# Optimization experiments

Measured on AMD Instinct MI355X. Metric: run time of the kernel, lower is better.

The kernel has to match this reference:

```python
import jax, jax.numpy as jnp
import numpy as np

REG_STD = jnp.asarray([0.1, 0.1, 0.2, 0.2, 0.1], dtype=jnp.float32)  # normalize() target_std, mean=0


def setup_inputs() -> dict:
    key = jax.random.key(0)
    ks = jax.random.split(key, 8)
    B, N, C, R = 2, 2048, 256, 7
    D, H, NCLS = C * R * R, 1024, 10
    features = jax.random.normal(ks[0], (B, N, C, R, R), jnp.float32)
    boxes = jax.random.uniform(ks[1], (B, N, 5), jnp.float32)  # cx,cy,w,h,angle (stride units)
    strides = jnp.ones((B, N, 5), jnp.float32)
    W1 = jax.random.normal(ks[2], (D, H), jnp.float32) * 0.02
    b1 = jnp.zeros((H,), jnp.float32)
    W2 = jax.random.normal(ks[3], (H, H), jnp.float32) * 0.02
    b2 = jnp.zeros((H,), jnp.float32)
    Wc = jax.random.normal(ks[4], (H, NCLS + 1), jnp.float32) * 0.02
    bc = jnp.zeros((NCLS + 1,), jnp.float32)
    Wr = jax.random.normal(ks[5], (H, 5), jnp.float32) * 0.02
    br = jnp.zeros((5,), jnp.float32)
    return {"features": features, "boxes": boxes, "strides": strides,
            "W1": W1, "b1": b1, "W2": W2, "b2": b2,
            "Wc": Wc, "bc": bc, "Wr": Wr, "br": br}


def reference(features, boxes, strides, W1, b1, W2, b2, Wc, bc, Wr, br):
    B, N = features.shape[:2]
    x = features.reshape(B, N, -1)                      # [B,N,C*7*7] (Flatten start_dim=2)
    h = jax.nn.relu(jnp.einsum('bnd,dh->bnh', x, W1) + b1)
    h = jax.nn.relu(jnp.einsum('bnh,hk->bnk', h, W2) + b2)
    classification = jnp.einsum('bnh,hc->bnc', h, Wc) + bc   # [B,N,num_classes+1]
    regression = (jnp.einsum('bnh,hr->bnr', h, Wr) + br) * REG_STD  # normalize: mean 0, std per-channel
    # rois: proposal boxes scaled back to image coords (all but angle)
    rois = boxes.at[..., :4].multiply(strides[..., :4])
    # box decode (delta-style for x,y; exp for w,h,angle)
    bx = boxes[..., 2] * regression[..., 0] + boxes[..., 0]
    by = boxes[..., 3] * regression[..., 1] + boxes[..., 1]
    bw = boxes[..., 2] * jnp.exp(regression[..., 2])
    bh = boxes[..., 3] * jnp.exp(regression[..., 3])
    ba = boxes[..., 4] * jnp.exp(regression[..., 4])
    dec = jnp.stack((bx, by, bw, bh, ba), axis=-1)
    dec = dec.at[..., :4].multiply(strides[..., :4])
    return classification, dec, rois
```

## Files before the change

kernel.cpp:

```cpp
#include <hip/hip_runtime.h>
#include <hip/hip_bf16.h>
#include <stdint.h>

typedef unsigned short u16;
typedef unsigned int u32;
typedef float f32x4 __attribute__((ext_vector_type(4)));
typedef short bf16x8 __attribute__((ext_vector_type(8)));

#define DEV static __device__ __forceinline__

DEV u16 f2bf(float x) {
    u32 u = __float_as_uint(x);
    u32 r = (u + 0x7fffu + ((u >> 16) & 1u)) >> 16;
    return (u16)r;
}
DEV float bf2f(u16 u) { return __uint_as_float(((u32)u) << 16); }


__global__ __launch_bounds__(256) void k_cvt_bf16(const float* __restrict__ in,
                                                  u16* __restrict__ out, int n8) {
    int i = blockIdx.x * 256 + threadIdx.x;
    if (i >= n8) return;
    const float4* p = (const float4*)in + (size_t)i * 2;
    float4 a = p[0], b = p[1];
    u16 r[8];
    r[0] = f2bf(a.x); r[1] = f2bf(a.y); r[2] = f2bf(a.z); r[3] = f2bf(a.w);
    r[4] = f2bf(b.x); r[5] = f2bf(b.y); r[6] = f2bf(b.z); r[7] = f2bf(b.w);
    *(uint4*)(out + (size_t)i * 8) = *(const uint4*)r;
}

__global__ __launch_bounds__(256) void k_transpose_cvt(const float* __restrict__ in,
                                                       u16* __restrict__ out,
                                                       int K, int N) {
    __shared__ float tile[32][33];
    int tiles_n = N >> 5;
    int tk = blockIdx.x / tiles_n, tn = blockIdx.x % tiles_n;
    int tx = threadIdx.x & 31, ty = threadIdx.x >> 5;
    int k0 = tk * 32, n0 = tn * 32;
#pragma unroll
    for (int i = 0; i < 4; ++i)
        tile[ty * 4 + i][tx] = in[(size_t)(k0 + ty * 4 + i) * N + n0 + tx];
    __syncthreads();
#pragma unroll
    for (int i = 0; i < 4; ++i)
        out[(size_t)(n0 + ty * 4 + i) * K + k0 + tx] = f2bf(tile[tx][ty * 4 + i]);
}

__global__ __launch_bounds__(256) void k_pack_head(const float* __restrict__ Wc,
                                                   const float* __restrict__ Wr,
                                                   float* __restrict__ Whead) {
    int r = blockIdx.x * 256 + threadIdx.x;
    if (r >= 1024) return;
    float* o = Whead + (size_t)r * 16;
#pragma unroll
    for (int c = 0; c < 11; ++c) o[c] = Wc[(size_t)r * 11 + c];
#pragma unroll
    for (int c = 0; c < 5; ++c) o[11 + c] = Wr[(size_t)r * 5 + c];
}

__global__ __launch_bounds__(256) void k_gemm_bias_relu(
    const u16* __restrict__ A, const u16* __restrict__ Bt,
    const float* __restrict__ bias, u16* __restrict__ C,
    int M, int N, int K) {
    __shared__ u16 As[128 * 64];
    __shared__ u16 Bs[64 * 64];

    int nwg = gridDim.x;
    int cpx = nwg >> 3;
    int bid = blockIdx.x;
    int swz = (bid & 7) * cpx + (bid >> 3);
    int ntn = N >> 6;
    int bm = swz / ntn, bn = swz % ntn;

    int tid = threadIdx.x;
    int lane = tid & 63, wid = tid >> 6;
    int wm = wid >> 1, wn = wid & 1;
    const int tm0 = bm * 128, tn0 = bn * 64;

    const int l8 = lane >> 3, l7 = lane & 7;

    f32x4 acc[4][2] = {};

    int kt = K >> 6;
    for (int t = 0; t < kt; ++t) {
        int k0 = t << 6;
#pragma unroll
        for (int i = 0; i < 4; ++i) {
            int seg = wid * 4 + i;
            const u16* g = A + (size_t)(tm0 + seg * 8 + l8) * K + k0 + l7 * 8;
            __builtin_amdgcn_global_load_lds(
                (const __attribute__((address_space(1))) u32*)g,
                (__attribute__((address_space(3))) u32*)&As[seg * 512], 16, 0, 0);
        }
#pragma unroll
        for (int i = 0; i < 2; ++i) {
            int seg = wid * 2 + i;
            const u16* g = Bt + (size_t)(tn0 + seg * 8 + l8) * K + k0 + l7 * 8;
            __builtin_amdgcn_global_load_lds(
                (const __attribute__((address_space(1))) u32*)g,
                (__attribute__((address_space(3))) u32*)&Bs[seg * 512], 16, 0, 0);
        }
        __syncthreads();

#pragma unroll
        for (int kk = 0; kk < 2; ++kk) {
            int kc = kk * 32 + (lane >> 4) * 8;
            bf16x8 a[4], b[2];
#pragma unroll
            for (int m = 0; m < 4; ++m)
                a[m] = *(const bf16x8*)&As[(wm * 64 + m * 16 + (lane & 15)) * 64 + kc];
#pragma unroll
            for (int n = 0; n < 2; ++n)
                b[n] = *(const bf16x8*)&Bs[(wn * 32 + n * 16 + (lane & 15)) * 64 + kc];
#pragma unroll
            for (int m = 0; m < 4; ++m)
#pragma unroll
                for (int n = 0; n < 2; ++n)
                    acc[m][n] = __builtin_amdgcn_mfma_f32_16x16x32_bf16(
                        a[m], b[n], acc[m][n], 0, 0, 0);
        }
        __syncthreads();
    }

    int cr = lane >> 4, cc = lane & 15;
#pragma unroll
    for (int n = 0; n < 2; ++n) {
        int col = tn0 + wn * 32 + n * 16 + cc;
        float bv = bias[col];
#pragma unroll
        for (int m = 0; m < 4; ++m) {
            int row0 = tm0 + wm * 64 + m * 16 + cr * 4;
#pragma unroll
            for (int r = 0; r < 4; ++r) {
                float v = fmaxf(acc[m][n][r] + bv, 0.0f);
                C[(size_t)(row0 + r) * N + col] = f2bf(v);
            }
        }
    }
}

__global__ __launch_bounds__(256) void k_head(
    const u16* __restrict__ h2, const float* __restrict__ Whead,
    const float* __restrict__ bc, const float* __restrict__ br,
    const float* __restrict__ boxes, const float* __restrict__ strides,
    float* __restrict__ cls_out, float* __restrict__ dec_out,
    float* __restrict__ rois_out) {
    int lane = threadIdx.x & 63;
    int row = blockIdx.x * 4 + (threadIdx.x >> 6);

    const u16* hr = h2 + (size_t)row * 1024;
    float acc[16];
#pragma unroll
    for (int i = 0; i < 16; ++i) acc[i] = 0.0f;

#pragma unroll
    for (int j = 0; j < 16; ++j) {
        int k = j * 64 + lane;
        float h = bf2f(hr[k]);
        const float4* wp = (const float4*)(Whead + (size_t)k * 16);
        float4 q0 = wp[0], q1 = wp[1], q2 = wp[2], q3 = wp[3];
        acc[0]  = fmaf(h, q0.x, acc[0]);  acc[1]  = fmaf(h, q0.y, acc[1]);
        acc[2]  = fmaf(h, q0.z, acc[2]);  acc[3]  = fmaf(h, q0.w, acc[3]);
        acc[4]  = fmaf(h, q1.x, acc[4]);  acc[5]  = fmaf(h, q1.y, acc[5]);
        acc[6]  = fmaf(h, q1.z, acc[6]);  acc[7]  = fmaf(h, q1.w, acc[7]);
        acc[8]  = fmaf(h, q2.x, acc[8]);  acc[9]  = fmaf(h, q2.y, acc[9]);
        acc[10] = fmaf(h, q2.z, acc[10]); acc[11] = fmaf(h, q2.w, acc[11]);
        acc[12] = fmaf(h, q3.x, acc[12]); acc[13] = fmaf(h, q3.y, acc[13]);
        acc[14] = fmaf(h, q3.z, acc[14]); acc[15] = fmaf(h, q3.w, acc[15]);
    }
#pragma unroll
    for (int i = 0; i < 16; ++i) {
#pragma unroll
        for (int off = 32; off > 0; off >>= 1)
            acc[i] += __shfl_xor(acc[i], off);
    }

    if (lane == 0) {
        float* co = cls_out + (size_t)row * 11;
#pragma unroll
        for (int c = 0; c < 11; ++c) co[c] = acc[c] + bc[c];

        const float STD[5] = {0.1f, 0.1f, 0.2f, 0.2f, 0.1f};
        float reg[5];
#pragma unroll
        for (int j = 0; j < 5; ++j) reg[j] = (acc[11 + j] + br[j]) * STD[j];

        const float* bx = boxes + (size_t)row * 5;
        const float* st = strides + (size_t)row * 5;
        float b0 = bx[0], b1 = bx[1], b2 = bx[2], b3 = bx[3], b4 = bx[4];
        float s0 = st[0], s1 = st[1], s2 = st[2], s3 = st[3];

        float dx = b2 * reg[0] + b0;
        float dy = b3 * reg[1] + b1;
        float dw = b2 * expf(reg[2]);
        float dh = b3 * expf(reg[3]);
        float da = b4 * expf(reg[4]);

        float* dd = dec_out + (size_t)row * 5;
        dd[0] = dx * s0; dd[1] = dy * s1; dd[2] = dw * s2; dd[3] = dh * s3; dd[4] = da;

        float* rr = rois_out + (size_t)row * 5;
        rr[0] = b0 * s0; rr[1] = b1 * s1; rr[2] = b2 * s2; rr[3] = b3 * s3; rr[4] = b4;
    }
}

extern "C" void kernel_launch(void* const* d_in, const int* in_sizes, int n_in,
                              void* d_out, int out_size, void* d_ws, size_t ws_size,
                              hipStream_t stream) {
    const float* features = (const float*)d_in[0];
    const float* boxes    = (const float*)d_in[1];
    const float* strides  = (const float*)d_in[2];
    const float* W1 = (const float*)d_in[3];
    const float* b1 = (const float*)d_in[4];
    const float* W2 = (const float*)d_in[5];
    const float* b2 = (const float*)d_in[6];
    const float* Wc = (const float*)d_in[7];
    const float* bc = (const float*)d_in[8];
    const float* Wr = (const float*)d_in[9];
    const float* br = (const float*)d_in[10];

    const int M = 4096;
    const int K = 12544;
    const int H = 1024;

    char* ws = (char*)d_ws;
    u16*   Abf   = (u16*)(ws + 0);
    u16*   W1T   = (u16*)(ws + 102760448);
    u16*   W2T   = (u16*)(ws + 128450560);
    float* Whead = (float*)(ws + 130547712);
    u16*   h1    = (u16*)(ws + 130613248);
    u16*   h2    = (u16*)(ws + 139001856);

    k_cvt_bf16<<<25088, 256, 0, stream>>>(features, Abf, 6422528);
    k_transpose_cvt<<<(K / 32) * (H / 32), 256, 0, stream>>>(W1, W1T, K, H);
    k_transpose_cvt<<<(H / 32) * (H / 32), 256, 0, stream>>>(W2, W2T, H, H);
    k_pack_head<<<4, 256, 0, stream>>>(Wc, Wr, Whead);

    k_gemm_bias_relu<<<(M / 128) * (H / 64), 256, 0, stream>>>(Abf, W1T, b1, h1, M, H, K);
    k_gemm_bias_relu<<<(M / 128) * (H / 64), 256, 0, stream>>>(h1, W2T, b2, h2, M, H, H);

    float* cls  = (float*)d_out;
    float* dec  = cls + (size_t)4096 * 11;
    float* rois = dec + (size_t)4096 * 5;
    k_head<<<1024, 256, 0, stream>>>(h2, Whead, bc, br, boxes, strides, cls, dec, rois);
}
```

Measured before the change: 628.2 us.

## Fuse fp32-to-bf16 feature conversion into split-K GEMM1 with swizzled LDS

Removes the separate pass that converts the 100MB fp32 feature tensor to bf16. GEMM1 now loads fp32 features directly and converts them in registers with a packed bf16 instruction. GEMM1 is split along K into two halves, writing fp32 partial results that a new combine kernel sums with bias and ReLU, which doubles the number of workgroups. LDS tiles in both GEMMs use an XOR swizzle to reduce bank conflicts. The cost is an extra partial-sum buffer round trip, and the A loads become synchronous register loads instead of direct-to-LDS loads.

```diff
diff --git a/kernel.cpp b/kernel.cpp
--- a/kernel.cpp
+++ b/kernel.cpp
@@ -15,19 +15,12 @@
     return (u16)r;
 }
 DEV float bf2f(u16 u) { return __uint_as_float(((u32)u) << 16); }
-
-
-__global__ __launch_bounds__(256) void k_cvt_bf16(const float* __restrict__ in,
-                                                  u16* __restrict__ out, int n8) {
-    int i = blockIdx.x * 256 + threadIdx.x;
-    if (i >= n8) return;
-    const float4* p = (const float4*)in + (size_t)i * 2;
-    float4 a = p[0], b = p[1];
-    u16 r[8];
-    r[0] = f2bf(a.x); r[1] = f2bf(a.y); r[2] = f2bf(a.z); r[3] = f2bf(a.w);
-    r[4] = f2bf(b.x); r[5] = f2bf(b.y); r[6] = f2bf(b.z); r[7] = f2bf(b.w);
-    *(uint4*)(out + (size_t)i * 8) = *(const uint4*)r;
-}
+DEV u32 pk2bf(float lo, float hi) {
+    u32 r;
+    asm("v_cvt_pk_bf16_f32 %0, %1, %2" : "=v"(r) : "v"(lo), "v"(hi));
+    return r;
+}
+
 
 __global__ __launch_bounds__(256) void k_transpose_cvt(const float* __restrict__ in,
                                                        u16* __restrict__ out,
@@ -58,7 +51,130 @@
     for (int c = 0; c < 5; ++c) o[11 + c] = Wr[(size_t)r * 5 + c];
 }
 
-__global__ __launch_bounds__(256) void k_gemm_bias_relu(
+__global__ __launch_bounds__(256, 4) void k_gemm1(
+    const float* __restrict__ A, const u16* __restrict__ Bt,
+    float* __restrict__ P, int M, int N, int K, int KHALF) {
+    __shared__ u16 As[128 * 64];
+    __shared__ u16 Bs[64 * 64];
+
+    int nwg = gridDim.x;
+    int cpx = nwg >> 3;
+    int bid = blockIdx.x;
+    int swz = (bid & 7) * cpx + (bid >> 3);
+    int split = swz >> 9;
+    int tile = swz & 511;
+    int bm = tile >> 4, bn = tile & 15;
+
+    int tid = threadIdx.x;
+    int lane = tid & 63, wid = tid >> 6;
+    int wm = wid >> 1, wn = wid & 1;
+    const int tm0 = bm * 128, tn0 = bn * 64;
+    const int kbeg = split * KHALF;
+
+    const int l8 = lane >> 3, l7 = lane & 7;
+    const int bsrc = ((l7 ^ l8) << 3);
+
+    f32x4 acc[4][2] = {};
+
+    int kt = KHALF >> 6;
+    for (int t = 0; t < kt; ++t) {
+        int k0 = kbeg + (t << 6);
+#pragma unroll
+        for (int i = 0; i < 2; ++i) {
+            int seg = wid * 2 + i;
+            const u16* g = Bt + (size_t)(tn0 + seg * 8 + l8) * K + k0 + bsrc;
+            __builtin_amdgcn_global_load_lds(
+                (const __attribute__((address_space(1))) u32*)g,
+                (__attribute__((address_space(3))) u32*)&Bs[seg * 512], 16, 0, 0);
+        }
+#pragma unroll
+        for (int h = 0; h < 2; ++h) {
+            float4 fa[2][2];
+#pragma unroll
+            for (int i = 0; i < 2; ++i) {
+                int s = (h * 2 + i) * 256 + tid;
+                int r = s >> 3, cg = s & 7;
+                const float* g = A + (size_t)(tm0 + r) * K + k0 + cg * 8;
+                fa[i][0] = *(const float4*)g;
+                fa[i][1] = *(const float4*)(g + 4);
+            }
+#pragma unroll
+            for (int i = 0; i < 2; ++i) {
+                int s = (h * 2 + i) * 256 + tid;
+                int r = s >> 3, cg = s & 7;
+                u32 pk[4];
+                pk[0] = pk2bf(fa[i][0].x, fa[i][0].y);
+                pk[1] = pk2bf(fa[i][0].z, fa[i][0].w);
+                pk[2] = pk2bf(fa[i][1].x, fa[i][1].y);
+                pk[3] = pk2bf(fa[i][1].z, fa[i][1].w);
+                int cb = (cg << 4) ^ ((r & 7) << 4);
+                *(uint4*)((char*)As + r * 128 + cb) = *(const uint4*)pk;
+            }
+        }
+        __syncthreads();
+
+#pragma unroll
+        for (int kk = 0; kk < 2; ++kk) {
+            int cb = (kk << 6) + ((lane >> 4) << 4);
+            bf16x8 a[4], b[2];
+#pragma unroll
+            for (int m = 0; m < 4; ++m) {
+                int r = wm * 64 + m * 16 + (lane & 15);
+                a[m] = *(const bf16x8*)((const char*)As + r * 128 + (cb ^ ((r & 7) << 4)));
+            }
+#pragma unroll
+            for (int n = 0; n < 2; ++n) {
+                int r = wn * 32 + n * 16 + (lane & 15);
+                b[n] = *(const bf16x8*)((const char*)Bs + r * 128 + (cb ^ ((r & 7) << 4)));
+            }
+#pragma unroll
+            for (int m = 0; m < 4; ++m)
+#pragma unroll
+                for (int n = 0; n < 2; ++n)
+                    acc[m][n] = __builtin_amdgcn_mfma_f32_16x16x32_bf16(
+                        a[m], b[n], acc[m][n], 0, 0, 0);
+        }
+        __syncthreads();
+    }
+
+    float* Ps = P + (size_t)split * M * N;
+    int cr = lane >> 4, cc = lane & 15;
+#pragma unroll
+    for (int n = 0; n < 2; ++n) {
+        int col = tn0 + wn * 32 + n * 16 + cc;
+#pragma unroll
+        for (int m = 0; m < 4; ++m) {
+            int row0 = tm0 + wm * 64 + m * 16 + cr * 4;
+#pragma unroll
+            for (int r = 0; r < 4; ++r)
+                Ps[(size_t)(row0 + r) * N + col] = acc[m][n][r];
+        }
+    }
+}
+
+__global__ __launch_bounds__(256) void k_combine(const float* __restrict__ P,
+                                                 const float* __restrict__ bias,
+                                                 u16* __restrict__ out,
+                                                 int MN, int N) {
+    int i = blockIdx.x * 256 + threadIdx.x;
+    int ncol8 = N >> 3;
+    int row = i / ncol8, c8 = i - row * ncol8;
+    size_t off = (size_t)row * N + (size_t)c8 * 8;
+    const float4* p0 = (const float4*)(P + off);
+    const float4* p1 = (const float4*)(P + (size_t)MN + off);
+    const float4* bp = (const float4*)(bias + (size_t)c8 * 8);
+    float4 a0 = p0[0], a1 = p0[1];
+    float4 b0 = p1[0], b1 = p1[1];
+    float4 q0 = bp[0], q1 = bp[1];
+    float v0 = fmaxf(a0.x + b0.x + q0.x, 0.f), v1 = fmaxf(a0.y + b0.y + q0.y, 0.f);
+    float v2 = fmaxf(a0.z + b0.z + q0.z, 0.f), v3 = fmaxf(a0.w + b0.w + q0.w, 0.f);
+    float v4 = fmaxf(a1.x + b1.x + q1.x, 0.f), v5 = fmaxf(a1.y + b1.y + q1.y, 0.f);
+    float v6 = fmaxf(a1.z + b1.z + q1.z, 0.f), v7 = fmaxf(a1.w + b1.w + q1.w, 0.f);
+    u32 pk[4] = {pk2bf(v0, v1), pk2bf(v2, v3), pk2bf(v4, v5), pk2bf(v6, v7)};
+    *(uint4*)(out + off) = *(const uint4*)pk;
+}
+
+__global__ __launch_bounds__(256) void k_gemm2(
     const u16* __restrict__ A, const u16* __restrict__ Bt,
     const float* __restrict__ bias, u16* __restrict__ C,
     int M, int N, int K) {
@@ -78,6 +194,7 @@
     const int tm0 = bm * 128, tn0 = bn * 64;
 
     const int l8 = lane >> 3, l7 = lane & 7;
+    const int bsrc = ((l7 ^ l8) << 3);
 
     f32x4 acc[4][2] = {};
 
@@ -87,7 +204,7 @@
 #pragma unroll
         for (int i = 0; i < 4; ++i) {
             int seg = wid * 4 + i;
-            const u16* g = A + (size_t)(tm0 + seg * 8 + l8) * K + k0 + l7 * 8;
+            const u16* g = A + (size_t)(tm0 + seg * 8 + l8) * K + k0 + bsrc;
             __builtin_amdgcn_global_load_lds(
                 (const __attribute__((address_space(1))) u32*)g,
                 (__attribute__((address_space(3))) u32*)&As[seg * 512], 16, 0, 0);
@@ -95,7 +212,7 @@
 #pragma unroll
         for (int i = 0; i < 2; ++i) {
             int seg = wid * 2 + i;
-            const u16* g = Bt + (size_t)(tn0 + seg * 8 + l8) * K + k0 + l7 * 8;
+            const u16* g = Bt + (size_t)(tn0 + seg * 8 + l8) * K + k0 + bsrc;
             __builtin_amdgcn_global_load_lds(
                 (const __attribute__((address_space(1))) u32*)g,
                 (__attribute__((address_space(3))) u32*)&Bs[seg * 512], 16, 0, 0);
@@ -104,14 +221,18 @@
 
 #pragma unroll
         for (int kk = 0; kk < 2; ++kk) {
-            int kc = kk * 32 + (lane >> 4) * 8;
+            int cb = (kk << 6) + ((lane >> 4) << 4);
             bf16x8 a[4], b[2];
 #pragma unroll
-            for (int m = 0; m < 4; ++m)
-                a[m] = *(const bf16x8*)&As[(wm * 64 + m * 16 + (lane & 15)) * 64 + kc];
-#pragma unroll
-            for (int n = 0; n < 2; ++n)
-                b[n] = *(const bf16x8*)&Bs[(wn * 32 + n * 16 + (lane & 15)) * 64 + kc];
+            for (int m = 0; m < 4; ++m) {
+                int r = wm * 64 + m * 16 + (lane & 15);
+                a[m] = *(const bf16x8*)((const char*)As + r * 128 + (cb ^ ((r & 7) << 4)));
+            }
+#pragma unroll
+            for (int n = 0; n < 2; ++n) {
+                int r = wn * 32 + n * 16 + (lane & 15);
+                b[n] = *(const bf16x8*)((const char*)Bs + r * 128 + (cb ^ ((r & 7) << 4)));
+            }
 #pragma unroll
             for (int m = 0; m < 4; ++m)
 #pragma unroll
@@ -224,20 +345,20 @@
     const int H = 1024;
 
     char* ws = (char*)d_ws;
-    u16*   Abf   = (u16*)(ws + 0);
-    u16*   W1T   = (u16*)(ws + 102760448);
-    u16*   W2T   = (u16*)(ws + 128450560);
-    float* Whead = (float*)(ws + 130547712);
-    u16*   h1    = (u16*)(ws + 130613248);
-    u16*   h2    = (u16*)(ws + 139001856);
-
-    k_cvt_bf16<<<25088, 256, 0, stream>>>(features, Abf, 6422528);
+    u16*   W1T   = (u16*)(ws + 0);
+    u16*   W2T   = (u16*)(ws + 25690112);
+    float* Whead = (float*)(ws + 27787264);
+    float* P     = (float*)(ws + 27852800);
+    u16*   h1    = (u16*)(ws + 61407232);
+    u16*   h2    = (u16*)(ws + 69795840);
+
     k_transpose_cvt<<<(K / 32) * (H / 32), 256, 0, stream>>>(W1, W1T, K, H);
     k_transpose_cvt<<<(H / 32) * (H / 32), 256, 0, stream>>>(W2, W2T, H, H);
     k_pack_head<<<4, 256, 0, stream>>>(Wc, Wr, Whead);
 
-    k_gemm_bias_relu<<<(M / 128) * (H / 64), 256, 0, stream>>>(Abf, W1T, b1, h1, M, H, K);
-    k_gemm_bias_relu<<<(M / 128) * (H / 64), 256, 0, stream>>>(h1, W2T, b2, h2, M, H, H);
+    k_gemm1<<<1024, 256, 0, stream>>>(features, W1T, P, M, H, K, K / 2);
+    k_combine<<<(M * H / 8) / 256, 256, 0, stream>>>(P, b1, h1, M * H, H);
+    k_gemm2<<<(M / 128) * (H / 64), 256, 0, stream>>>(h1, W2T, b2, h2, M, H, H);
 
     float* cls  = (float*)d_out;
     float* dec  = cls + (size_t)4096 * 11;
```

After: 616.2 us. No clear change (-1.9%).

## Double-buffer GEMM LDS tiles with XOR swizzle and packed bf16 conversion

Applied to the files above, without the earlier changes.

Adds a two-stage LDS ping-pong to the bias+ReLU GEMM so the next K-tile's global-to-LDS loads are issued before the current tile's MFMAs. LDS rows are XOR-swizzled at 16-byte granularity to cut bank conflicts on fragment reads. Launch bounds request two blocks per CU. The fp32-to-bf16 conversion kernel now uses the hardware packed convert instruction. Doubling LDS per block may limit occupancy.

```diff
diff --git a/kernel.cpp b/kernel.cpp
--- a/kernel.cpp
+++ b/kernel.cpp
@@ -15,6 +15,11 @@
     return (u16)r;
 }
 DEV float bf2f(u16 u) { return __uint_as_float(((u32)u) << 16); }
+DEV u32 pk2bf(float lo, float hi) {
+    u32 r;
+    asm("v_cvt_pk_bf16_f32 %0, %1, %2" : "=v"(r) : "v"(lo), "v"(hi));
+    return r;
+}
 
 
 __global__ __launch_bounds__(256) void k_cvt_bf16(const float* __restrict__ in,
@@ -23,10 +28,8 @@
     if (i >= n8) return;
     const float4* p = (const float4*)in + (size_t)i * 2;
     float4 a = p[0], b = p[1];
-    u16 r[8];
-    r[0] = f2bf(a.x); r[1] = f2bf(a.y); r[2] = f2bf(a.z); r[3] = f2bf(a.w);
-    r[4] = f2bf(b.x); r[5] = f2bf(b.y); r[6] = f2bf(b.z); r[7] = f2bf(b.w);
-    *(uint4*)(out + (size_t)i * 8) = *(const uint4*)r;
+    u32 pk[4] = {pk2bf(a.x, a.y), pk2bf(a.z, a.w), pk2bf(b.x, b.y), pk2bf(b.z, b.w)};
+    *(uint4*)(out + (size_t)i * 8) = *(const uint4*)pk;
 }
 
 __global__ __launch_bounds__(256) void k_transpose_cvt(const float* __restrict__ in,
@@ -58,12 +61,12 @@
     for (int c = 0; c < 5; ++c) o[11 + c] = Wr[(size_t)r * 5 + c];
 }
 
-__global__ __launch_bounds__(256) void k_gemm_bias_relu(
+__global__ __launch_bounds__(256, 2) void k_gemm_bias_relu(
     const u16* __restrict__ A, const u16* __restrict__ Bt,
     const float* __restrict__ bias, u16* __restrict__ C,
     int M, int N, int K) {
-    __shared__ u16 As[128 * 64];
-    __shared__ u16 Bs[64 * 64];
+    __shared__ u16 As[2][128 * 64];
+    __shared__ u16 Bs[2][64 * 64];
 
     int nwg = gridDim.x;
     int cpx = nwg >> 3;
@@ -78,40 +81,53 @@
     const int tm0 = bm * 128, tn0 = bn * 64;
 
     const int l8 = lane >> 3, l7 = lane & 7;
-
-    f32x4 acc[4][2] = {};
-
-    int kt = K >> 6;
-    for (int t = 0; t < kt; ++t) {
-        int k0 = t << 6;
+    const int bsrc = ((l7 ^ l8) << 3);
+
+    auto stage = [&](u16* as, u16* bs, int k0) {
 #pragma unroll
         for (int i = 0; i < 4; ++i) {
             int seg = wid * 4 + i;
-            const u16* g = A + (size_t)(tm0 + seg * 8 + l8) * K + k0 + l7 * 8;
+            const u16* g = A + (size_t)(tm0 + seg * 8 + l8) * K + k0 + bsrc;
             __builtin_amdgcn_global_load_lds(
                 (const __attribute__((address_space(1))) u32*)g,
-                (__attribute__((address_space(3))) u32*)&As[seg * 512], 16, 0, 0);
+                (__attribute__((address_space(3))) u32*)(as + seg * 512), 16, 0, 0);
         }
 #pragma unroll
         for (int i = 0; i < 2; ++i) {
             int seg = wid * 2 + i;
-            const u16* g = Bt + (size_t)(tn0 + seg * 8 + l8) * K + k0 + l7 * 8;
+            const u16* g = Bt + (size_t)(tn0 + seg * 8 + l8) * K + k0 + bsrc;
             __builtin_amdgcn_global_load_lds(
                 (const __attribute__((address_space(1))) u32*)g,
-                (__attribute__((address_space(3))) u32*)&Bs[seg * 512], 16, 0, 0);
-        }
-        __syncthreads();
-
+                (__attribute__((address_space(3))) u32*)(bs + seg * 512), 16, 0, 0);
+        }
+    };
+
+    f32x4 acc[4][2] = {};
+
+    int kt = K >> 6;
+    stage(As[0], Bs[0], 0);
+    __syncthreads();
+
+    int cur = 0;
+    for (int t = 0; t < kt; ++t) {
+        if (t + 1 < kt) stage(As[cur ^ 1], Bs[cur ^ 1], (t + 1) << 6);
+
+        const u16* as = As[cur];
+        const u16* bs = Bs[cur];
 #pragma unroll
         for (int kk = 0; kk < 2; ++kk) {
-            int kc = kk * 32 + (lane >> 4) * 8;
+            int cb = (kk << 6) + ((lane >> 4) << 4);
             bf16x8 a[4], b[2];
 #pragma unroll
-            for (int m = 0; m < 4; ++m)
-                a[m] = *(const bf16x8*)&As[(wm * 64 + m * 16 + (lane & 15)) * 64 + kc];
-#pragma unroll
-            for (int n = 0; n < 2; ++n)
-                b[n] = *(const bf16x8*)&Bs[(wn * 32 + n * 16 + (lane & 15)) * 64 + kc];
+            for (int m = 0; m < 4; ++m) {
+                int r = wm * 64 + m * 16 + (lane & 15);
+                a[m] = *(const bf16x8*)((const char*)as + r * 128 + (cb ^ ((r & 7) << 4)));
+            }
+#pragma unroll
+            for (int n = 0; n < 2; ++n) {
+                int r = wn * 32 + n * 16 + (lane & 15);
+                b[n] = *(const bf16x8*)((const char*)bs + r * 128 + (cb ^ ((r & 7) << 4)));
+            }
 #pragma unroll
             for (int m = 0; m < 4; ++m)
 #pragma unroll
@@ -120,6 +136,7 @@
                         a[m], b[n], acc[m][n], 0, 0, 0);
         }
         __syncthreads();
+        cur ^= 1;
     }
 
     int cr = lane >> 4, cc = lane & 15;
```

Result: faster. 595.7 us (-5.2%).
